# Kernel tuning notes

Measured on AMD Instinct MI355X. Metric: run time of the kernel, lower is better.

Reference implementation:

```python
import jax, jax.numpy as jnp
import numpy as np

D_V, D_Q, D_H = 256, 128, 64

def setup_inputs() -> dict:
    key = jax.random.key(0)
    ks = jax.random.split(key, 8)
    B, T = 512, 512
    query = jax.random.normal(ks[0], (B, D_Q), dtype=jnp.float32)
    values = jax.random.normal(ks[1], (B, T, D_V), dtype=jnp.float32)
    s1 = 1.0 / np.sqrt(D_V)
    s2 = 1.0 / np.sqrt(D_Q)
    sv = 1.0 / np.sqrt(D_H)
    W1 = jax.random.uniform(ks[2], (D_H, D_V), jnp.float32, -s1, s1)
    b1 = jax.random.uniform(ks[3], (D_H,), jnp.float32, -s1, s1)
    W2 = jax.random.uniform(ks[4], (D_H, D_Q), jnp.float32, -s2, s2)
    b2 = jax.random.uniform(ks[5], (D_H,), jnp.float32, -s2, s2)
    Wv = jax.random.uniform(ks[6], (1, D_H), jnp.float32, -sv, sv)
    bv = jax.random.uniform(ks[7], (1,), jnp.float32, -sv, sv)
    return {"query": query, "values": values, "W1": W1, "b1": b1,
            "W2": W2, "b2": b2, "Wv": Wv, "bv": bv}

def reference(query, values, W1, b1, W2, b2, Wv, bv):
    # hidden_with_time_axis: [B,1,128]
    h = jnp.einsum('btv,hv->bth', values, W1) + b1 \
        + (jnp.einsum('bq,hq->bh', query, W2) + b2)[:, None, :]   # [B,T,64]
    score = jnp.einsum('bth,oh->bto', jnp.tanh(h), Wv) + bv        # [B,T,1]
    attention_weights = jax.nn.softmax(score, axis=0)              # softmax over dim 0, as written
    context_vector = jnp.sum(attention_weights * values, axis=0)   # [T,256]
    return (context_vector, attention_weights)
```

## Files before the change

kernel.cpp:

```cpp
#include <hip/hip_runtime.h>
#include <hip/hip_bf16.h>

#define Tt 512
#define Bb 512
#define DV 256
#define DQ 128
#define DH 64
#define CTXN (Tt * DV)
#define TW 64
#define BCH 8
#define NCH (Bb / BCH)

typedef __attribute__((ext_vector_type(8))) short bf16x8;
typedef __attribute__((ext_vector_type(4))) float f32x4;

__device__ __forceinline__ unsigned short f2bf(float x) {
  unsigned u = __float_as_uint(x);
  u += 0x7FFFu + ((u >> 16) & 1u);
  return (unsigned short)(u >> 16);
}

__global__ void prep_kernel(const float* __restrict__ query,
                            const float* __restrict__ W1,
                            const float* __restrict__ W2,
                            const float* __restrict__ b1,
                            const float* __restrict__ b2,
                            float* __restrict__ qh,
                            unsigned short* __restrict__ w1bf) {
  __shared__ float q[DQ];
  const int blk = blockIdx.x;
  const int h = threadIdx.x;
  if (blk < Bb) {
    q[h]      = query[blk * DQ + h];
    q[h + 64] = query[blk * DQ + h + 64];
    __syncthreads();
    const float* w2r = W2 + h * DQ;
    float acc = 0.f;
#pragma unroll 8
    for (int k = 0; k < DQ; ++k) acc = fmaf(w2r[k], q[k], acc);
    qh[blk * DH + h] = acc + b1[h] + b2[h];
  } else {
    int base = (blk - Bb) * 256;
#pragma unroll
    for (int k = 0; k < 4; ++k) {
      int i = base + (k << 6) + h;
      w1bf[i] = f2bf(W1[i]);
    }
  }
}

__global__ __launch_bounds__(256, 2) void fused3_kernel(
    const float* __restrict__ values,
    const unsigned short* __restrict__ w1bf,
    const float* __restrict__ qh,
    const float* __restrict__ Wv,
    const float* __restrict__ bv,
    float* __restrict__ es,
    float* __restrict__ num_p,
    float* __restrict__ den_p) {
  __shared__ __align__(16) unsigned short lB[DH * DV];
  __shared__ float lQh[BCH * DH];
  const int tid = threadIdx.x;
  const int chunk = blockIdx.x & (NCH - 1);
  const int t0 = (blockIdx.x >> 6) * TW;
  const int b0 = chunk * BCH;

  const uint4* w1v = (const uint4*)w1bf;
#pragma unroll
  for (int i = 0; i < 8; ++i) {
    int vec = i * 256 + tid;
    uint4 d = w1v[vec];
    int row = vec >> 5;
    int u = vec & 31;
    int byte = (row << 9) + (u << 4);
    *(uint4*)((char*)lB + (byte ^ ((row & 7) << 4))) = d;
  }
  lQh[tid]       = qh[b0 * DH + tid];
  lQh[tid + 256] = qh[b0 * DH + tid + 256];
  __syncthreads();

  const int wv = tid >> 6, lane = tid & 63;
  const int lrow = lane & 15, g = lane >> 4;
  const int arow = wv * 16 + lrow;

  float wvc[4];
#pragma unroll
  for (int nt = 0; nt < 4; ++nt) wvc[nt] = Wv[nt * 16 + lrow];
  const float bv0 = bv[0];

  float num[8][8];
#pragma unroll
  for (int ks = 0; ks < 8; ++ks)
#pragma unroll
    for (int e = 0; e < 8; ++e) num[ks][e] = 0.f;
  float den = 0.f;

#pragma unroll 1
  for (int bi = 0; bi < BCH; ++bi) {
    const int b = b0 + bi;
    const float* ap = values + ((size_t)b * Tt + t0 + arow) * DV + g * 8;

    f32x4 acc[4];
#pragma unroll
    for (int nt = 0; nt < 4; ++nt) acc[nt] = (f32x4){0.f, 0.f, 0.f, 0.f};
#pragma unroll
    for (int ks = 0; ks < 8; ++ks) {
      float4 f0 = *(const float4*)(ap + ks * 32);
      float4 f1 = *(const float4*)(ap + ks * 32 + 4);
      bf16x8 af;
      af[0] = (short)f2bf(f0.x); af[1] = (short)f2bf(f0.y);
      af[2] = (short)f2bf(f0.z); af[3] = (short)f2bf(f0.w);
      af[4] = (short)f2bf(f1.x); af[5] = (short)f2bf(f1.y);
      af[6] = (short)f2bf(f1.z); af[7] = (short)f2bf(f1.w);
      int k2 = (ks * 32 + g * 8) * 2;
#pragma unroll
      for (int nt = 0; nt < 4; ++nt) {
        int brow = nt * 16 + lrow;
        bf16x8 bf = *(const bf16x8*)((const char*)lB +
                                     (((brow << 9) + k2) ^ ((brow & 7) << 4)));
        acc[nt] = __builtin_amdgcn_mfma_f32_16x16x32_bf16(af, bf, acc[nt], 0, 0, 0);
      }
    }

    const float* qrow = lQh + bi * DH;
    float sc[4] = {0.f, 0.f, 0.f, 0.f};
#pragma unroll
    for (int nt = 0; nt < 4; ++nt) {
      float qv = qrow[nt * 16 + lrow];
#pragma unroll
      for (int j = 0; j < 4; ++j) {
        float hv = acc[nt][j] + qv;
        float e2 = __expf(2.f * hv);
        float th = (e2 - 1.f) / (e2 + 1.f);
        sc[j] = fmaf(th, wvc[nt], sc[j]);
      }
    }
#pragma unroll
    for (int j = 0; j < 4; ++j) {
      float v = sc[j];
      v += __shfl_xor(v, 1);
      v += __shfl_xor(v, 2);
      v += __shfl_xor(v, 4);
      v += __shfl_xor(v, 8);
      sc[j] = __expf(v + bv0);
    }
    if (lrow == 0) {
#pragma unroll
      for (int j = 0; j < 4; ++j)
        es[(size_t)b * Tt + t0 + wv * 16 + g * 4 + j] = sc[j];
    }
    int src = (lrow >> 2) << 4;
    float w0 = __shfl(sc[0], src), w1 = __shfl(sc[1], src);
    float w2 = __shfl(sc[2], src), w3 = __shfl(sc[3], src);
    int jm = lrow & 3;
    float w = (jm == 0) ? w0 : (jm == 1) ? w1 : (jm == 2) ? w2 : w3;
    den += w;
#pragma unroll
    for (int ks = 0; ks < 8; ++ks) {
      float4 v0 = *(const float4*)(ap + ks * 32);
      float4 v1 = *(const float4*)(ap + ks * 32 + 4);
      num[ks][0] = fmaf(w, v0.x, num[ks][0]);
      num[ks][1] = fmaf(w, v0.y, num[ks][1]);
      num[ks][2] = fmaf(w, v0.z, num[ks][2]);
      num[ks][3] = fmaf(w, v0.w, num[ks][3]);
      num[ks][4] = fmaf(w, v1.x, num[ks][4]);
      num[ks][5] = fmaf(w, v1.y, num[ks][5]);
      num[ks][6] = fmaf(w, v1.z, num[ks][6]);
      num[ks][7] = fmaf(w, v1.w, num[ks][7]);
    }
  }

  float* np = num_p + ((size_t)chunk * Tt + t0 + arow) * DV + g * 8;
#pragma unroll
  for (int ks = 0; ks < 8; ++ks) {
    *(float4*)(np + ks * 32) =
        make_float4(num[ks][0], num[ks][1], num[ks][2], num[ks][3]);
    *(float4*)(np + ks * 32 + 4) =
        make_float4(num[ks][4], num[ks][5], num[ks][6], num[ks][7]);
  }
  if (g == 0) den_p[chunk * Tt + t0 + arow] = den;
}

__global__ __launch_bounds__(256) void fin_ctx_kernel(
    const float* __restrict__ num_p, const float* __restrict__ den_p,
    float* __restrict__ Zbuf, float* __restrict__ out) {
  const int t = blockIdx.x;
  const int tid = threadIdx.x;
  float Z = 0.f;
#pragma unroll 16
  for (int c = 0; c < NCH; ++c) Z += den_p[c * Tt + t];
  float s = 0.f;
#pragma unroll 8
  for (int c = 0; c < NCH; ++c)
    s += num_p[((size_t)c * Tt + t) * DV + tid];
  out[t * DV + tid] = s / Z;
  if (tid == 0) Zbuf[t] = Z;
}

__global__ __launch_bounds__(256) void fin_w_kernel(
    const float* __restrict__ es, const float* __restrict__ Zbuf,
    float* __restrict__ out) {
  const int b = blockIdx.x;
  const int tid = threadIdx.x;
#pragma unroll
  for (int i = 0; i < 2; ++i) {
    int t = i * 256 + tid;
    out[CTXN + b * Tt + t] = es[(size_t)b * Tt + t] / Zbuf[t];
  }
}

extern "C" void kernel_launch(void* const* d_in, const int* in_sizes, int n_in,
                              void* d_out, int out_size, void* d_ws, size_t ws_size,
                              hipStream_t stream) {
  const float* query  = (const float*)d_in[0];
  const float* values = (const float*)d_in[1];
  const float* W1     = (const float*)d_in[2];
  const float* b1     = (const float*)d_in[3];
  const float* W2     = (const float*)d_in[4];
  const float* b2     = (const float*)d_in[5];
  const float* Wv     = (const float*)d_in[6];
  const float* bv     = (const float*)d_in[7];
  float* out = (float*)d_out;
  char* ws = (char*)d_ws;
  float* qh            = (float*)ws;
  unsigned short* w1bf = (unsigned short*)(ws + 131072);
  float* es            = (float*)(ws + 163840);
  float* den_p         = (float*)(ws + 1212416);
  float* Zbuf          = (float*)(ws + 1343488);
  float* num_p         = (float*)(ws + 1345536);

  prep_kernel<<<dim3(Bb + 64), dim3(64), 0, stream>>>(query, W1, W2, b1, b2, qh, w1bf);
  fused3_kernel<<<dim3(512), dim3(256), 0, stream>>>(values, w1bf, qh, Wv, bv,
                                                     es, num_p, den_p);
  fin_ctx_kernel<<<dim3(Tt), dim3(256), 0, stream>>>(num_p, den_p, Zbuf, out);
  fin_w_kernel<<<dim3(Bb), dim3(256), 0, stream>>>(es, Zbuf, out);
}
```

Baseline: 119.1 us.

## Halve batch chunk, merge finalize kernels, and use rcp-based tanh

Batch chunk per block drops from 8 to 4, doubling the fused grid to 1024 blocks, and launch bounds rise to 3 blocks per SM for more parallelism and latency hiding. Partial denominators are stored transposed so each t's partials are contiguous and read as float4. The two finalize kernels become one, with each weight block recomputing Z itself instead of going through a Zbuf, which removes a launch and a dependency. The cost is twice as much num_p partial traffic in the reduction. tanh now uses a hardware reciprocal instead of a divide, which saves ALU work with slightly lower precision.

Result: slower. 243.3 us (+104.3%).

```diff
diff --git a/kernel.cpp b/kernel.cpp
--- a/kernel.cpp
+++ b/kernel.cpp
@@ -8,7 +8,7 @@
 #define DH 64
 #define CTXN (Tt * DV)
 #define TW 64
-#define BCH 8
+#define BCH 4
 #define NCH (Bb / BCH)
 
 typedef __attribute__((ext_vector_type(8))) short bf16x8;
@@ -49,7 +49,7 @@
   }
 }
 
-__global__ __launch_bounds__(256, 2) void fused3_kernel(
+__global__ __launch_bounds__(256, 3) void fused4_kernel(
     const float* __restrict__ values,
     const unsigned short* __restrict__ w1bf,
     const float* __restrict__ qh,
@@ -62,7 +62,7 @@
   __shared__ float lQh[BCH * DH];
   const int tid = threadIdx.x;
   const int chunk = blockIdx.x & (NCH - 1);
-  const int t0 = (blockIdx.x >> 6) * TW;
+  const int t0 = (blockIdx.x >> 7) * TW;
   const int b0 = chunk * BCH;
 
   const uint4* w1v = (const uint4*)w1bf;
@@ -75,8 +75,7 @@
     int byte = (row << 9) + (u << 4);
     *(uint4*)((char*)lB + (byte ^ ((row & 7) << 4))) = d;
   }
-  lQh[tid]       = qh[b0 * DH + tid];
-  lQh[tid + 256] = qh[b0 * DH + tid + 256];
+  lQh[tid] = qh[b0 * DH + tid];
   __syncthreads();
 
   const int wv = tid >> 6, lane = tid & 63;
@@ -131,7 +130,7 @@
       for (int j = 0; j < 4; ++j) {
         float hv = acc[nt][j] + qv;
         float e2 = __expf(2.f * hv);
-        float th = (e2 - 1.f) / (e2 + 1.f);
+        float th = 1.f - 2.f * __builtin_amdgcn_rcpf(e2 + 1.f);
         sc[j] = fmaf(th, wvc[nt], sc[j]);
       }
     }
@@ -178,34 +177,42 @@
     *(float4*)(np + ks * 32 + 4) =
         make_float4(num[ks][4], num[ks][5], num[ks][6], num[ks][7]);
   }
-  if (g == 0) den_p[chunk * Tt + t0 + arow] = den;
-}
-
-__global__ __launch_bounds__(256) void fin_ctx_kernel(
+  if (g == 0) den_p[(t0 + arow) * NCH + chunk] = den;
+}
+
+__global__ __launch_bounds__(256) void fin_kernel(
     const float* __restrict__ num_p, const float* __restrict__ den_p,
-    float* __restrict__ Zbuf, float* __restrict__ out) {
-  const int t = blockIdx.x;
+    const float* __restrict__ es, float* __restrict__ out) {
+  const int blk = blockIdx.x;
   const int tid = threadIdx.x;
-  float Z = 0.f;
-#pragma unroll 16
-  for (int c = 0; c < NCH; ++c) Z += den_p[c * Tt + t];
-  float s = 0.f;
+  if (blk < Tt) {
+    const int t = blk;
+    float Z = 0.f;
+    const float4* dp = (const float4*)(den_p + t * NCH);
+#pragma unroll
+    for (int i = 0; i < NCH / 4; ++i) {
+      float4 d = dp[i];
+      Z += (d.x + d.y) + (d.z + d.w);
+    }
+    float s = 0.f;
 #pragma unroll 8
-  for (int c = 0; c < NCH; ++c)
-    s += num_p[((size_t)c * Tt + t) * DV + tid];
-  out[t * DV + tid] = s / Z;
-  if (tid == 0) Zbuf[t] = Z;
-}
-
-__global__ __launch_bounds__(256) void fin_w_kernel(
-    const float* __restrict__ es, const float* __restrict__ Zbuf,
-    float* __restrict__ out) {
-  const int b = blockIdx.x;
-  const int tid = threadIdx.x;
-#pragma unroll
-  for (int i = 0; i < 2; ++i) {
-    int t = i * 256 + tid;
-    out[CTXN + b * Tt + t] = es[(size_t)b * Tt + t] / Zbuf[t];
+    for (int c = 0; c < NCH; ++c)
+      s += num_p[((size_t)c * Tt + t) * DV + tid];
+    out[t * DV + tid] = s / Z;
+  } else {
+    const int b = blk - Tt;
+#pragma unroll
+    for (int i = 0; i < 2; ++i) {
+      const int t = i * 256 + tid;
+      float Z = 0.f;
+      const float4* dp = (const float4*)(den_p + t * NCH);
+#pragma unroll
+      for (int k = 0; k < NCH / 4; ++k) {
+        float4 d = dp[k];
+        Z += (d.x + d.y) + (d.z + d.w);
+      }
+      out[CTXN + b * Tt + t] = es[(size_t)b * Tt + t] / Z;
+    }
   }
 }
 
@@ -226,12 +233,10 @@
   unsigned short* w1bf = (unsigned short*)(ws + 131072);
   float* es            = (float*)(ws + 163840);
   float* den_p         = (float*)(ws + 1212416);
-  float* Zbuf          = (float*)(ws + 1343488);
-  float* num_p         = (float*)(ws + 1345536);
+  float* num_p         = (float*)(ws + (size_t)2 * 1024 * 1024);
 
   prep_kernel<<<dim3(Bb + 64), dim3(64), 0, stream>>>(query, W1, W2, b1, b2, qh, w1bf);
-  fused3_kernel<<<dim3(512), dim3(256), 0, stream>>>(values, w1bf, qh, Wv, bv,
-                                                     es, num_p, den_p);
-  fin_ctx_kernel<<<dim3(Tt), dim3(256), 0, stream>>>(num_p, den_p, Zbuf, out);
-  fin_w_kernel<<<dim3(Bb), dim3(256), 0, stream>>>(es, Zbuf, out);
-}
+  fused4_kernel<<<dim3(1024), dim3(256), 0, stream>>>(values, w1bf, qh, Wv, bv,
+                                                      es, num_p, den_p);
+  fin_kernel<<<dim3(1024), dim3(256), 0, stream>>>(num_p, den_p, es, out);
+}
```
